# Kernel optimization log

Hardware: AMD Instinct MI355X
Metric: run time of the kernel (lower is better)

The kernel has to match this reference:

```python
import jax, jax.numpy as jnp
import numpy as np

N_HEADS = 16
SCALE = 8.0  # sqrt(inner_dim // n_heads) = sqrt(64), scale='inv_sqrt'


def setup_inputs() -> dict:
    key = jax.random.key(0)
    k1, k2, k3, k4 = jax.random.split(key, 4)
    b, n, d_model, inner = 8, 2048, 1024, 1024
    x = jax.random.normal(k1, (b, n, d_model), dtype=jnp.float32)
    Wqkv = jax.random.normal(k2, (3 * inner, d_model), dtype=jnp.float32) * (1.0 / np.sqrt(d_model))
    Wproj = jax.random.normal(k3, (d_model, inner), dtype=jnp.float32) * (1.0 / np.sqrt(inner))
    bproj = jax.random.normal(k4, (d_model,), dtype=jnp.float32) * 0.01
    return {"x": x, "Wqkv": Wqkv, "Wproj": Wproj, "bproj": bproj}


def reference(x, Wqkv, Wproj, bproj):
    b, n, _ = x.shape
    qkv = jnp.einsum('bnm,fm->bnf', x, Wqkv)          # [b, n, 3*inner]
    qkv = qkv.reshape(b, n, N_HEADS, -1)              # [b, n, h, 3*dh] (einops 'b n (h d)')
    dh = qkv.shape[3] // 3
    q, k, v = qkv[..., :dh], qkv[..., dh:2 * dh], qkv[..., 2 * dh:]
    # Faithful to source: q @ k.transpose(-1,-2) on [b,n,h,dh] -> scores over HEADS, [b,n,h,h]
    scores = jnp.einsum('bnhd,bngd->bnhg', q, k) / SCALE
    attn = jax.nn.softmax(scores, axis=-1)            # softmax over last head axis
    out = jnp.einsum('bnhg,bngd->bnhd', attn, v)      # [b, n, h, dh]
    out = out.reshape(b, n, -1)                       # [b, n, inner]
    return jnp.einsum('bni,mi->bnm', out, Wproj) + bproj
```

## Files before the change

kernel.cpp:

```cpp
#include <hip/hip_runtime.h>
#include <stdint.h>

typedef __bf16 bf16_t;
typedef __bf16 bf16x8 __attribute__((ext_vector_type(8)));
typedef float f32x4 __attribute__((ext_vector_type(4)));

__device__ __forceinline__ void gload_lds16(const void* g, void* l) {
  __builtin_amdgcn_global_load_lds(
      (const __attribute__((address_space(1))) uint32_t*)g,
      (__attribute__((address_space(3))) uint32_t*)l, 16, 0, 0);
}

__global__ void cast3_f32_bf16(const float* __restrict__ a, bf16_t* __restrict__ ao, int n4a,
                               const float* __restrict__ b, bf16_t* __restrict__ bo, int n4b,
                               const float* __restrict__ c, bf16_t* __restrict__ co, int n4c) {
  int i = blockIdx.x * blockDim.x + threadIdx.x;
  int stride = gridDim.x * blockDim.x;
  int total = n4a + n4b + n4c;
  for (int idx = i; idx < total; idx += stride) {
    const float* src; bf16_t* dst; int j = idx;
    if (j < n4a) { src = a; dst = ao; }
    else if ((j -= n4a) < n4b) { src = b; dst = bo; }
    else { j -= n4b; src = c; dst = co; }
    float4 v = reinterpret_cast<const float4*>(src)[j];
    union { bf16_t b[4]; uint2 u; } pk;
    pk.b[0] = (bf16_t)v.x; pk.b[1] = (bf16_t)v.y;
    pk.b[2] = (bf16_t)v.z; pk.b[3] = (bf16_t)v.w;
    reinterpret_cast<uint2*>(dst)[j] = pk.u;
  }
}

template <bool BF16_OUT>
__global__ __launch_bounds__(512, 2)
void gemm_8ph(const bf16_t* __restrict__ A, const bf16_t* __restrict__ B,
              void* __restrict__ Cout, const float* __restrict__ bias, int N) {
  constexpr int K = 1024, NI = 8;
  __shared__ bf16_t Al[2][2][128 * 64];
  __shared__ bf16_t Bl[2][2][128 * 64];

  const int tid = threadIdx.x;
  const int l = tid & 63, w = tid >> 6;
  const int wm = w >> 2, wn = w & 3;

  const int bid = blockIdx.x;
  const int xcd = bid & 7, idx = bid >> 3;
  const int bx = xcd * 8 + (idx & 7);
  const int by = idx >> 3;
  const int m0 = bx * 256, n0 = by * 256;

  const int srow = tid >> 3;
  const int sca = ((tid & 7) ^ (srow & 7)) * 8;
  const bf16_t* pA = A + (size_t)(m0 + srow) * K + sca;
  const bf16_t* pB = B + (size_t)(n0 + srow) * K + sca;

#define ST_A(t_, d_, h_) do {                                                         \
    gload_lds16(pA + (size_t)((h_) * 128) * K + (t_) * 64, &Al[d_][h_][tid * 8]);     \
    gload_lds16(pA + (size_t)((h_) * 128 + 64) * K + (t_) * 64,                       \
                &Al[d_][h_][4096 + tid * 8]); } while (0)
#define ST_B(t_, d_, h_) do {                                                         \
    gload_lds16(pB + (size_t)((h_) * 128) * K + (t_) * 64, &Bl[d_][h_][tid * 8]);     \
    gload_lds16(pB + (size_t)((h_) * 128 + 64) * K + (t_) * 64,                       \
                &Bl[d_][h_][4096 + tid * 8]); } while (0)

  const int arow = l & 15;
  const int brow = (wn & 1) * 64 + (l & 15);
  const int cks0 = (((l >> 4) + 0) ^ (l & 7)) * 8;
  const int cks1 = (((l >> 4) + 4) ^ (l & 7)) * 8;

#define LDA4(dst, base, i0) do {                                                      \
    _Pragma("unroll") for (int i = 0; i < 4; ++i) {                                   \
      dst[i][0] = *reinterpret_cast<const bf16x8*>(&base[(arow + (i0 + i) * 16) * 64 + cks0]); \
      dst[i][1] = *reinterpret_cast<const bf16x8*>(&base[(arow + (i0 + i) * 16) * 64 + cks1]); \
    } } while (0)
#define LDB2(dst, base, j0) do {                                                      \
    _Pragma("unroll") for (int j = 0; j < 2; ++j) {                                   \
      dst[j][0] = *reinterpret_cast<const bf16x8*>(&base[(brow + (j0 + j) * 16) * 64 + cks0]); \
      dst[j][1] = *reinterpret_cast<const bf16x8*>(&base[(brow + (j0 + j) * 16) * 64 + cks1]); \
    } } while (0)

#define MM16(afr, bfr, I0, J0)                                                        \
    __builtin_amdgcn_s_setprio(1);                                                    \
    _Pragma("unroll") for (int i = 0; i < 4; ++i)                                     \
    _Pragma("unroll") for (int j = 0; j < 2; ++j)                                     \
    _Pragma("unroll") for (int s = 0; s < 2; ++s)                                     \
      acc[I0 + i][J0 + j] = __builtin_amdgcn_mfma_f32_16x16x32_bf16(                  \
          afr[i][s], bfr[j][s], acc[I0 + i][J0 + j], 0, 0, 0);                        \
    __builtin_amdgcn_s_setprio(0);

#define BARF() do { asm volatile("" ::: "memory");                                    \
                    __builtin_amdgcn_s_barrier();                                     \
                    asm volatile("" ::: "memory"); } while (0)

  f32x4 acc[8][4] = {};

  ST_A(0, 0, 0); ST_A(0, 0, 1); ST_B(0, 0, 0); ST_B(0, 0, 1);
  ST_B(1, 1, 0); ST_B(1, 1, 1);
  asm volatile("s_waitcnt vmcnt(4)" ::: "memory");
  BARF();

  for (int it = 0; it < NI; ++it) {
    const bool last = (it == NI - 1);
    const int ta = 2 * it, tb = ta + 1;
    const bf16_t* As0 = &Al[0][wm][0];
    const bf16_t* Bs0 = &Bl[0][wn >> 1][0];
    const bf16_t* As1 = &Al[1][wm][0];
    const bf16_t* Bs1 = &Bl[1][wn >> 1][0];
    bf16x8 af0[4][2], af1[4][2], bf0[2][2], bf1[2][2];

    LDB2(bf0, Bs0, 0); LDA4(af0, As0, 0);
    ST_A(tb, 1, 0);
    BARF();
    MM16(af0, bf0, 0, 0);
    BARF();
    LDB2(bf1, Bs0, 2);
    ST_A(tb, 1, 1);
    BARF();
    MM16(af0, bf1, 0, 2);
    BARF();
    LDA4(af1, As0, 4);
    if (!last) ST_B(ta + 2, 0, 0);
    BARF();
    MM16(af1, bf0, 4, 0);
    BARF();
    if (!last) ST_B(ta + 2, 0, 1);
    BARF();
    MM16(af1, bf1, 4, 2);
    if (last) asm volatile("s_waitcnt vmcnt(0)" ::: "memory");
    else      asm volatile("s_waitcnt vmcnt(4)" ::: "memory");
    BARF();

    LDB2(bf0, Bs1, 0); LDA4(af0, As1, 0);
    if (!last) ST_A(ta + 2, 0, 0);
    BARF();
    MM16(af0, bf0, 0, 0);
    BARF();
    LDB2(bf1, Bs1, 2);
    if (!last) ST_A(ta + 2, 0, 1);
    BARF();
    MM16(af0, bf1, 0, 2);
    BARF();
    LDA4(af1, As1, 4);
    if (!last) ST_B(tb + 2, 1, 0);
    BARF();
    MM16(af1, bf0, 4, 0);
    BARF();
    if (!last) ST_B(tb + 2, 1, 1);
    BARF();
    MM16(af1, bf1, 4, 2);
    if (!last) asm volatile("s_waitcnt vmcnt(4)" ::: "memory");
    BARF();
  }
#undef ST_A
#undef ST_B
#undef LDA4
#undef LDB2
#undef MM16
#undef BARF

  const int r0 = m0 + wm * 128 + (l >> 4) * 4;
  const int c0 = n0 + wn * 64 + (l & 15);
  if (BF16_OUT) {
    bf16_t* C = (bf16_t*)Cout;
#pragma unroll
    for (int i = 0; i < 8; ++i)
#pragma unroll
      for (int j = 0; j < 4; ++j)
#pragma unroll
        for (int r = 0; r < 4; ++r)
          C[(size_t)(r0 + i * 16 + r) * N + (c0 + j * 16)] = (bf16_t)acc[i][j][r];
  } else {
    float* C = (float*)Cout;
#pragma unroll
    for (int i = 0; i < 8; ++i)
#pragma unroll
      for (int j = 0; j < 4; ++j)
#pragma unroll
        for (int r = 0; r < 4; ++r)
          C[(size_t)(r0 + i * 16 + r) * N + (c0 + j * 16)] =
              acc[i][j][r] + bias[c0 + j * 16];
  }
}

__global__ __launch_bounds__(256)
void attn_heads(const bf16_t* __restrict__ qkv, bf16_t* __restrict__ out) {
  __shared__ float s[4][3072];
  const int w = threadIdx.x >> 6, l = threadIdx.x & 63;
  const size_t t = (size_t)blockIdx.x * 4 + w;
  const bf16_t* src = qkv + t * 3072;
#pragma unroll
  for (int i = 0; i < 6; ++i) {
    int f = (i * 64 + l) * 8;
    bf16x8 v = *reinterpret_cast<const bf16x8*>(&src[f]);
#pragma unroll
    for (int jj = 0; jj < 8; ++jj) s[w][f + jj] = (float)v[jj];
  }
  __syncthreads();

  const int h = l >> 2, ss = l & 3;
  float qr[16];
  const float* qb = &s[w][h * 192 + ss * 16];
#pragma unroll
  for (int d = 0; d < 16; ++d) qr[d] = qb[d];

  float sc[16];
#pragma unroll
  for (int g = 0; g < 16; ++g) {
    const float* kk = &s[w][g * 192 + 64 + ss * 16];
    float p = 0.f;
#pragma unroll
    for (int d = 0; d < 16; ++d) p += qr[d] * kk[d];
    p += __shfl_xor(p, 1);
    p += __shfl_xor(p, 2);
    sc[g] = p * 0.125f;
  }
  float m = sc[0];
#pragma unroll
  for (int g = 1; g < 16; ++g) m = fmaxf(m, sc[g]);
  float sum = 0.f;
#pragma unroll
  for (int g = 0; g < 16; ++g) { sc[g] = __expf(sc[g] - m); sum += sc[g]; }
  float inv = 1.f / sum;

  float o[16] = {};
#pragma unroll
  for (int g = 0; g < 16; ++g) {
    float a = sc[g] * inv;
    const float* vv = &s[w][g * 192 + 128 + ss * 16];
#pragma unroll
    for (int d = 0; d < 16; ++d) o[d] += a * vv[d];
  }
  union { bf16_t b[16]; uint4 u[2]; } pk;
#pragma unroll
  for (int d = 0; d < 16; ++d) pk.b[d] = (bf16_t)o[d];
  uint4* dst = reinterpret_cast<uint4*>(out + t * 1024 + h * 64 + ss * 16);
  dst[0] = pk.u[0];
  dst[1] = pk.u[1];
}

extern "C" void kernel_launch(void* const* d_in, const int* in_sizes, int n_in,
                              void* d_out, int out_size, void* d_ws, size_t ws_size,
                              hipStream_t stream) {
  const float* x     = (const float*)d_in[0];
  const float* Wqkv  = (const float*)d_in[1];
  const float* Wproj = (const float*)d_in[2];
  const float* bproj = (const float*)d_in[3];
  float* out = (float*)d_out;

  const int M = 8 * 2048;
  const int DM = 1024;
  const int F = 3072;

  char* ws = (char*)d_ws;
  bf16_t* xb     = (bf16_t*)ws;  ws += (size_t)M * DM * 2;
  bf16_t* wqkvb  = (bf16_t*)ws;  ws += (size_t)F * DM * 2;
  bf16_t* wprojb = (bf16_t*)ws;  ws += (size_t)DM * DM * 2;
  bf16_t* qkvb   = (bf16_t*)ws;  ws += (size_t)M * F * 2;
  bf16_t* attnb  = (bf16_t*)ws;

  cast3_f32_bf16<<<2048, 256, 0, stream>>>(x, xb, M * DM / 4,
                                           Wqkv, wqkvb, F * DM / 4,
                                           Wproj, wprojb, DM * DM / 4);

  gemm_8ph<true><<<(M / 256) * (F / 256), 512, 0, stream>>>(
      xb, wqkvb, (void*)qkvb, nullptr, F);

  attn_heads<<<M / 4, 256, 0, stream>>>(qkvb, attnb);

  gemm_8ph<false><<<(M / 256) * (DM / 256), 512, 0, stream>>>(
      attnb, wprojb, (void*)out, bproj, DM);
}
```

Before: 202.4 us.

## Shrink GEMM block tile to 256x128 with 4 waves and K-step 32

Replaces the 512-thread 256x256 GEMM with a 256-thread kernel computing 256x128 tiles, using 32-wide K steps (16 double-buffered iterations) and a new LDS swizzle. It also drops half the barriers per phase so LDS fragment reads and MFMAs run without a barrier between them. The grid doubles in block count and shared memory per block drops, which targets occupancy and per-step sync overhead. The trade-off is lower reuse per loaded tile and more loop iterations with smaller MFMA batches.

Result: slower. 219.4 us (+8.4%).

```diff
diff --git a/kernel.cpp b/kernel.cpp
--- a/kernel.cpp
+++ b/kernel.cpp
@@ -31,130 +31,115 @@
 }
 
 template <bool BF16_OUT>
-__global__ __launch_bounds__(512, 2)
-void gemm_8ph(const bf16_t* __restrict__ A, const bf16_t* __restrict__ B,
-              void* __restrict__ Cout, const float* __restrict__ bias, int N) {
-  constexpr int K = 1024, NI = 8;
-  __shared__ bf16_t Al[2][2][128 * 64];
-  __shared__ bf16_t Bl[2][2][128 * 64];
+__global__ __launch_bounds__(256, 2)
+void gemm_3b(const bf16_t* __restrict__ A, const bf16_t* __restrict__ B,
+             void* __restrict__ Cout, const float* __restrict__ bias, int N) {
+  constexpr int K = 1024, NI = 16;
+  __shared__ bf16_t Al[2][2][128 * 32];
+  __shared__ bf16_t Bl[2][2][64 * 32];
 
   const int tid = threadIdx.x;
   const int l = tid & 63, w = tid >> 6;
-  const int wm = w >> 2, wn = w & 3;
+  const int wm = w >> 1, wn = w & 1;
 
   const int bid = blockIdx.x;
   const int xcd = bid & 7, idx = bid >> 3;
   const int bx = xcd * 8 + (idx & 7);
   const int by = idx >> 3;
-  const int m0 = bx * 256, n0 = by * 256;
-
-  const int srow = tid >> 3;
-  const int sca = ((tid & 7) ^ (srow & 7)) * 8;
+  const int m0 = bx * 256, n0 = by * 128;
+
+  const int srow = tid >> 2;
+  const int sca = ((tid & 3) ^ ((tid >> 3) & 3)) * 8;
   const bf16_t* pA = A + (size_t)(m0 + srow) * K + sca;
   const bf16_t* pB = B + (size_t)(n0 + srow) * K + sca;
 
-#define ST_A(t_, d_, h_) do {                                                         \
-    gload_lds16(pA + (size_t)((h_) * 128) * K + (t_) * 64, &Al[d_][h_][tid * 8]);     \
-    gload_lds16(pA + (size_t)((h_) * 128 + 64) * K + (t_) * 64,                       \
-                &Al[d_][h_][4096 + tid * 8]); } while (0)
-#define ST_B(t_, d_, h_) do {                                                         \
-    gload_lds16(pB + (size_t)((h_) * 128) * K + (t_) * 64, &Bl[d_][h_][tid * 8]);     \
-    gload_lds16(pB + (size_t)((h_) * 128 + 64) * K + (t_) * 64,                       \
-                &Bl[d_][h_][4096 + tid * 8]); } while (0)
-
-  const int arow = l & 15;
-  const int brow = (wn & 1) * 64 + (l & 15);
-  const int cks0 = (((l >> 4) + 0) ^ (l & 7)) * 8;
-  const int cks1 = (((l >> 4) + 4) ^ (l & 7)) * 8;
-
-#define LDA4(dst, base, i0) do {                                                      \
-    _Pragma("unroll") for (int i = 0; i < 4; ++i) {                                   \
-      dst[i][0] = *reinterpret_cast<const bf16x8*>(&base[(arow + (i0 + i) * 16) * 64 + cks0]); \
-      dst[i][1] = *reinterpret_cast<const bf16x8*>(&base[(arow + (i0 + i) * 16) * 64 + cks1]); \
-    } } while (0)
-#define LDB2(dst, base, j0) do {                                                      \
-    _Pragma("unroll") for (int j = 0; j < 2; ++j) {                                   \
-      dst[j][0] = *reinterpret_cast<const bf16x8*>(&base[(brow + (j0 + j) * 16) * 64 + cks0]); \
-      dst[j][1] = *reinterpret_cast<const bf16x8*>(&base[(brow + (j0 + j) * 16) * 64 + cks1]); \
-    } } while (0)
-
-#define MM16(afr, bfr, I0, J0)                                                        \
-    __builtin_amdgcn_s_setprio(1);                                                    \
-    _Pragma("unroll") for (int i = 0; i < 4; ++i)                                     \
-    _Pragma("unroll") for (int j = 0; j < 2; ++j)                                     \
-    _Pragma("unroll") for (int s = 0; s < 2; ++s)                                     \
-      acc[I0 + i][J0 + j] = __builtin_amdgcn_mfma_f32_16x16x32_bf16(                  \
-          afr[i][s], bfr[j][s], acc[I0 + i][J0 + j], 0, 0, 0);                        \
+#define ST_A(t_, d_, h_) do {                                                    \
+    gload_lds16(pA + (size_t)((h_) * 128) * K + (t_) * 32, &Al[d_][h_][tid * 8]); \
+    gload_lds16(pA + (size_t)((h_) * 128 + 64) * K + (t_) * 32,                  \
+                &Al[d_][h_][2048 + tid * 8]); } while (0)
+#define ST_B(t_, d_, h_) \
+    gload_lds16(pB + (size_t)((h_) * 64) * K + (t_) * 32, &Bl[d_][h_][tid * 8])
+
+  const int arow = (l & 15) * 32;
+  const int ck = ((l >> 4) ^ ((l >> 1) & 3)) * 8;
+
+#define RDA(dst, base, i0) do {                                                  \
+    _Pragma("unroll") for (int i = 0; i < 4; ++i)                                \
+      dst[i] = *reinterpret_cast<const bf16x8*>(&base[arow + ((i0) + i) * 512 + ck]); \
+  } while (0)
+#define RDB(dst, base, j0) do {                                                  \
+    _Pragma("unroll") for (int j = 0; j < 2; ++j)                                \
+      dst[j] = *reinterpret_cast<const bf16x8*>(&base[arow + ((j0) + j) * 512 + ck]); \
+  } while (0)
+
+#define MM8(afp, bfp, I0, J0)                                                    \
+    __builtin_amdgcn_s_setprio(1);                                               \
+    _Pragma("unroll") for (int i = 0; i < 4; ++i)                                \
+    _Pragma("unroll") for (int j = 0; j < 2; ++j)                                \
+      acc[(I0) + i][(J0) + j] = __builtin_amdgcn_mfma_f32_16x16x32_bf16(         \
+          afp[i], bfp[j], acc[(I0) + i][(J0) + j], 0, 0, 0);                     \
     __builtin_amdgcn_s_setprio(0);
 
-#define BARF() do { asm volatile("" ::: "memory");                                    \
-                    __builtin_amdgcn_s_barrier();                                     \
-                    asm volatile("" ::: "memory"); } while (0)
+#define BARF() do { asm volatile("" ::: "memory");  \
+    __builtin_amdgcn_s_barrier();                   \
+    asm volatile("" ::: "memory"); } while (0)
 
   f32x4 acc[8][4] = {};
+  bf16x8 aflo[4], afhi[4], bf01[2], bf23[2];
 
   ST_A(0, 0, 0); ST_A(0, 0, 1); ST_B(0, 0, 0); ST_B(0, 0, 1);
   ST_B(1, 1, 0); ST_B(1, 1, 1);
-  asm volatile("s_waitcnt vmcnt(4)" ::: "memory");
+  asm volatile("s_waitcnt vmcnt(2)" ::: "memory");
   BARF();
 
   for (int it = 0; it < NI; ++it) {
     const bool last = (it == NI - 1);
     const int ta = 2 * it, tb = ta + 1;
-    const bf16_t* As0 = &Al[0][wm][0];
-    const bf16_t* Bs0 = &Bl[0][wn >> 1][0];
-    const bf16_t* As1 = &Al[1][wm][0];
-    const bf16_t* Bs1 = &Bl[1][wn >> 1][0];
-    bf16x8 af0[4][2], af1[4][2], bf0[2][2], bf1[2][2];
-
-    LDB2(bf0, Bs0, 0); LDA4(af0, As0, 0);
+    const bf16_t* A0 = &Al[0][wm][0];
+    const bf16_t* B0 = &Bl[0][wn][0];
+    const bf16_t* A1 = &Al[1][wm][0];
+    const bf16_t* B1 = &Bl[1][wn][0];
+
+    RDB(bf01, B0, 0); RDA(aflo, A0, 0);
     ST_A(tb, 1, 0);
-    BARF();
-    MM16(af0, bf0, 0, 0);
-    BARF();
-    LDB2(bf1, Bs0, 2);
+    MM8(aflo, bf01, 0, 0);
+    BARF();
+    RDB(bf23, B0, 2);
     ST_A(tb, 1, 1);
-    BARF();
-    MM16(af0, bf1, 0, 2);
-    BARF();
-    LDA4(af1, As0, 4);
+    MM8(aflo, bf23, 0, 2);
+    BARF();
+    RDA(afhi, A0, 4);
     if (!last) ST_B(ta + 2, 0, 0);
-    BARF();
-    MM16(af1, bf0, 4, 0);
+    MM8(afhi, bf01, 4, 0);
     BARF();
     if (!last) ST_B(ta + 2, 0, 1);
-    BARF();
-    MM16(af1, bf1, 4, 2);
+    MM8(afhi, bf23, 4, 2);
     if (last) asm volatile("s_waitcnt vmcnt(0)" ::: "memory");
-    else      asm volatile("s_waitcnt vmcnt(4)" ::: "memory");
-    BARF();
-
-    LDB2(bf0, Bs1, 0); LDA4(af0, As1, 0);
+    else      asm volatile("s_waitcnt vmcnt(2)" ::: "memory");
+    BARF();
+
+    RDB(bf01, B1, 0); RDA(aflo, A1, 0);
     if (!last) ST_A(ta + 2, 0, 0);
-    BARF();
-    MM16(af0, bf0, 0, 0);
-    BARF();
-    LDB2(bf1, Bs1, 2);
+    MM8(aflo, bf01, 0, 0);
+    BARF();
+    RDB(bf23, B1, 2);
     if (!last) ST_A(ta + 2, 0, 1);
-    BARF();
-    MM16(af0, bf1, 0, 2);
-    BARF();
-    LDA4(af1, As1, 4);
+    MM8(aflo, bf23, 0, 2);
+    BARF();
+    RDA(afhi, A1, 4);
     if (!last) ST_B(tb + 2, 1, 0);
-    BARF();
-    MM16(af1, bf0, 4, 0);
+    MM8(afhi, bf01, 4, 0);
     BARF();
     if (!last) ST_B(tb + 2, 1, 1);
-    BARF();
-    MM16(af1, bf1, 4, 2);
-    if (!last) asm volatile("s_waitcnt vmcnt(4)" ::: "memory");
+    MM8(afhi, bf23, 4, 2);
+    if (!last) asm volatile("s_waitcnt vmcnt(2)" ::: "memory");
     BARF();
   }
 #undef ST_A
 #undef ST_B
-#undef LDA4
-#undef LDB2
-#undef MM16
+#undef RDA
+#undef RDB
+#undef MM8
 #undef BARF
 
   const int r0 = m0 + wm * 128 + (l >> 4) * 4;
@@ -261,11 +246,11 @@
                                            Wqkv, wqkvb, F * DM / 4,
                                            Wproj, wprojb, DM * DM / 4);
 
-  gemm_8ph<true><<<(M / 256) * (F / 256), 512, 0, stream>>>(
+  gemm_3b<true><<<(M / 256) * (F / 128), 256, 0, stream>>>(
       xb, wqkvb, (void*)qkvb, nullptr, F);
 
   attn_heads<<<M / 4, 256, 0, stream>>>(qkvb, attnb);
 
-  gemm_8ph<false><<<(M / 256) * (DM / 256), 512, 0, stream>>>(
+  gemm_3b<false><<<(M / 256) * (DM / 128), 256, 0, stream>>>(
       attnb, wprojb, (void*)out, bproj, DM);
 }
```
